# Optimization experiments

Hardware: AMD Instinct MI355X
Metric: run time of the kernel (lower is better)

Reference implementation:

```python
import jax, jax.numpy as jnp
import numpy as np

K_MSG = 1024   # message length k (rows of G)
N_CODE = 2048  # codeword length n (cols of G)
B = 32768      # number of message blocks


def setup_inputs() -> dict:
    key = jax.random.key(0)
    kb, kg = jax.random.split(key)
    b = jax.random.randint(kb, (B, K_MSG), 0, 2, dtype=jnp.int32)
    G = jax.random.randint(kg, (K_MSG, N_CODE), 0, 2, dtype=jnp.int32)
    return {"b": b, "G": G}


def reference(b, G):
    # GF(2) linear block encode: c = (b @ G) mod 2
    # b: [num_blocks, k] bits (0/1), G: [k, n] generator matrix (0/1)
    b2 = b.astype(jnp.int32)
    G2 = G.astype(jnp.int32)
    c = jnp.mod(jnp.matmul(b2, G2), 2)  # [num_blocks, n]
    return c.astype(jnp.int32)
```

## Files before the change

kernel.cpp:

```cpp
#include <hip/hip_runtime.h>
#include <stdint.h>

typedef unsigned int u32;
typedef unsigned long long u64;
typedef int v4i  __attribute__((ext_vector_type(4)));
typedef int v16i __attribute__((ext_vector_type(16)));

#define K_MSG   1024
#define N_CODE  2048
#define NB      32768

__global__ void pack_gBF(const int* __restrict__ G, u32* __restrict__ bf) {
    int idx = blockIdx.x * blockDim.x + threadIdx.x;
    const int j  = idx & (N_CODE - 1);
    const int kq = idx >> 11;
    u32 p = 0;
#pragma unroll
    for (int i = 0; i < 4; ++i) {
        int v = G[(size_t)(kq * 4 + i) * N_CODE + j];
        p |= (u32)(v & 1) << (8 * i);
    }
    const int jb = j >> 5, jr = j & 31;
    const int kb = kq >> 3, hi = (kq >> 2) & 1, b4 = kq & 3;
    bf[(size_t)(jb * 32 + kb) * 256 + hi * 128 + jr * 4 + b4] = p;
}


#define MFMA_I8(va, vb, vc) __builtin_amdgcn_mfma_i32_32x32x32_i8(va, vb, vc, 0, 0, 0)

#define MFMA_SET(sfx) do {                              \
    acc[0][0] = MFMA_I8(a0##sfx, b0##sfx, acc[0][0]);   \
    acc[0][1] = MFMA_I8(a0##sfx, b1##sfx, acc[0][1]);   \
    acc[0][2] = MFMA_I8(a0##sfx, b2##sfx, acc[0][2]);   \
    acc[0][3] = MFMA_I8(a0##sfx, b3##sfx, acc[0][3]);   \
    acc[1][0] = MFMA_I8(a1##sfx, b0##sfx, acc[1][0]);   \
    acc[1][1] = MFMA_I8(a1##sfx, b1##sfx, acc[1][1]);   \
    acc[1][2] = MFMA_I8(a1##sfx, b2##sfx, acc[1][2]);   \
    acc[1][3] = MFMA_I8(a1##sfx, b3##sfx, acc[1][3]);   \
} while (0)

#define LOAD_SET(sfx, s_) do {                                      \
    int ao_ = lr * 1024 + ((((s_) * 32) + hi * 16) ^ axor);         \
    a0##sfx = *(const v4i*)(As + ao_);                              \
    a1##sfx = *(const v4i*)(As + ao_ + 32768);                      \
    b0##sfx = *(const v4i*)(bp0 + (size_t)(s_) * 1024);             \
    b1##sfx = *(const v4i*)(bp1 + (size_t)(s_) * 1024);             \
    b2##sfx = *(const v4i*)(bp2 + (size_t)(s_) * 1024);             \
    b3##sfx = *(const v4i*)(bp3 + (size_t)(s_) * 1024);             \
} while (0)

#define EXPAND_ROW(pkp_, opp_, row_) do {                           \
    const u32 p0_ = (pkp_)[(row_) * 16 + (lane >> 3)];              \
    const u32 p1_ = (pkp_)[(row_) * 16 + 8 + (lane >> 3)];          \
    const int sb_ = (lane & 7) * 4;                                 \
    v4i v0_, v1_;                                                   \
    v0_.x = (int)((p0_ >> (sb_ + 0)) & 1u);                         \
    v0_.y = (int)((p0_ >> (sb_ + 1)) & 1u);                         \
    v0_.z = (int)((p0_ >> (sb_ + 2)) & 1u);                         \
    v0_.w = (int)((p0_ >> (sb_ + 3)) & 1u);                         \
    v1_.x = (int)((p1_ >> (sb_ + 0)) & 1u);                         \
    v1_.y = (int)((p1_ >> (sb_ + 1)) & 1u);                         \
    v1_.z = (int)((p1_ >> (sb_ + 2)) & 1u);                         \
    v1_.w = (int)((p1_ >> (sb_ + 3)) & 1u);                         \
    int* dst_ = (opp_) + (size_t)(row_) * N_CODE + lane * 4;        \
    *(v4i*)dst_         = v0_;                                      \
    *(v4i*)(dst_ + 256) = v1_;                                      \
} while (0)

__global__ __launch_bounds__(256, 2) void gemm_all(const int* __restrict__ b,
                                                   const char* __restrict__ bf,
                                                   int* __restrict__ out) {
    __shared__ __align__(16) char As[64 * 1024];
    __shared__ u32 pk[2][64 * 16];

    const int t   = threadIdx.x;
    const int bid = blockIdx.x;
    const int m0  = ((bid & 7) * 64 + (bid >> 3)) * 64;

    const int w = t >> 6, lane = t & 63, lr = lane & 31, hi = lane >> 5;
    const int axor = (lr & 7) << 4;

    {
        const int* src = b + (size_t)m0 * K_MSG;
#pragma unroll 8
        for (int i = 0; i < 64; ++i) {
            int4 v = *(const int4*)(src + (size_t)i * K_MSG + t * 4);
            u32 p = (u32)(v.x & 1) | ((u32)(v.y & 1) << 8) |
                    ((u32)(v.z & 1) << 16) | ((u32)(v.w & 1) << 24);
            *(u32*)(As + i * 1024 + ((t * 4) ^ ((i & 7) << 4))) = p;
        }
    }
    __syncthreads();

#pragma unroll 1
    for (int pass = 0; pass < 4; ++pass) {
        const int cur = pass & 1;
        const u32* pkp = pk[cur ^ 1];
        int* opp = out + (size_t)m0 * N_CODE + (pass - 1) * 512;

        const char* bp0 = bf + ((size_t)pass * 16 + w * 4) * 32768 + lane * 16;
        const char* bp1 = bp0 + 32768;
        const char* bp2 = bp0 + 65536;
        const char* bp3 = bp0 + 98304;

        v16i acc[2][4] = {};
        v4i a0A, a1A, b0A, b1A, b2A, b3A;
        v4i a0B, a1B, b0B, b1B, b2B, b3B;
        v4i a0C, a1C, b0C, b1C, b2C, b3C;
        v4i a0D, a1D, b0D, b1D, b2D, b3D;

        LOAD_SET(A, 0);
        LOAD_SET(B, 1);
#pragma unroll 1
        for (int s = 0; s < 32; s += 4) {
            LOAD_SET(C, s + 2);
            LOAD_SET(D, s + 3);
            MFMA_SET(A);
            MFMA_SET(B);
            if (s + 4 < 32) {
                LOAD_SET(A, s + 4);
                LOAD_SET(B, s + 5);
            }
            MFMA_SET(C);
            MFMA_SET(D);
            if (pass > 0) {
                const int row0 = w * 16 + (s >> 1);
                EXPAND_ROW(pkp, opp, row0);
                EXPAND_ROW(pkp, opp, row0 + 1);
            }
        }

        u32* pkc = pk[cur];
#pragma unroll
        for (int mi = 0; mi < 2; ++mi) {
#pragma unroll
            for (int ni = 0; ni < 4; ++ni) {
                const int cbL = w * 4 + ni;
#pragma unroll
                for (int r = 0; r < 16; ++r) {
                    u64 m = __ballot((acc[mi][ni][r] & 1) != 0);
                    if ((lane & 31) == r) {
                        const int row = mi * 32 + (r & 3) + 8 * (r >> 2) + 4 * hi;
                        pkc[row * 16 + cbL] = (u32)(m >> (hi * 32));
                    }
                }
            }
        }
        __syncthreads();
    }

    {
        const u32* pkp = pk[1];
        int* opp = out + (size_t)m0 * N_CODE + 3 * 512;
#pragma unroll 4
        for (int rr = 0; rr < 16; ++rr) {
            const int row = w * 16 + rr;
            EXPAND_ROW(pkp, opp, row);
        }
    }
}

__global__ void encode_naive(const int* __restrict__ b, const int* __restrict__ G,
                             int* __restrict__ out) {
    size_t idx = (size_t)blockIdx.x * blockDim.x + threadIdx.x;
    size_t total = (size_t)NB * N_CODE;
    if (idx >= total) return;
    int i = (int)(idx / N_CODE);
    int j = (int)(idx % N_CODE);
    int acc = 0;
    for (int k = 0; k < K_MSG; ++k)
        acc ^= b[(size_t)i * K_MSG + k] & G[(size_t)k * N_CODE + j];
    out[idx] = acc & 1;
}

extern "C" void kernel_launch(void* const* d_in, const int* in_sizes, int n_in,
                              void* d_out, int out_size, void* d_ws, size_t ws_size,
                              hipStream_t stream) {
    const int* b = (const int*)d_in[0];
    const int* G = (const int*)d_in[1];
    int* out = (int*)d_out;

    const size_t bf_bytes = (size_t)N_CODE * K_MSG;

    if (ws_size < bf_bytes) {
        size_t total = (size_t)NB * N_CODE;
        encode_naive<<<(unsigned)((total + 255) / 256), 256, 0, stream>>>(b, G, out);
        return;
    }

    char* bf = (char*)d_ws;

    pack_gBF<<<2048, 256, 0, stream>>>(G, (u32*)bf);
    gemm_all<<<NB / 64, 256, 0, stream>>>(b, bf, out);
}
```

Measured before the change: 134.6 us.

## Split N work across eight waves per block with smaller per-wave tiles

Doubles the block to 512 threads so each wave computes a 64x64 output slice instead of 64x128, halving accumulator and operand registers per wave. The main loop shrinks from quad-buffered to double-buffered loads, and the A staging and bit-expansion output work are redistributed across the eight waves. The aim is more resident waves to hide memory and MFMA latency. The cost is less A-fragment reuse per wave, hence more LDS reads per MFMA, and shallower software pipelining.

```diff
diff --git a/kernel.cpp b/kernel.cpp
--- a/kernel.cpp
+++ b/kernel.cpp
@@ -28,25 +28,19 @@
 
 #define MFMA_I8(va, vb, vc) __builtin_amdgcn_mfma_i32_32x32x32_i8(va, vb, vc, 0, 0, 0)
 
-#define MFMA_SET(sfx) do {                              \
+#define MFMAS(sfx) do {                                 \
     acc[0][0] = MFMA_I8(a0##sfx, b0##sfx, acc[0][0]);   \
     acc[0][1] = MFMA_I8(a0##sfx, b1##sfx, acc[0][1]);   \
-    acc[0][2] = MFMA_I8(a0##sfx, b2##sfx, acc[0][2]);   \
-    acc[0][3] = MFMA_I8(a0##sfx, b3##sfx, acc[0][3]);   \
     acc[1][0] = MFMA_I8(a1##sfx, b0##sfx, acc[1][0]);   \
     acc[1][1] = MFMA_I8(a1##sfx, b1##sfx, acc[1][1]);   \
-    acc[1][2] = MFMA_I8(a1##sfx, b2##sfx, acc[1][2]);   \
-    acc[1][3] = MFMA_I8(a1##sfx, b3##sfx, acc[1][3]);   \
 } while (0)
 
-#define LOAD_SET(sfx, s_) do {                                      \
+#define LOADS(sfx, s_) do {                                         \
     int ao_ = lr * 1024 + ((((s_) * 32) + hi * 16) ^ axor);         \
     a0##sfx = *(const v4i*)(As + ao_);                              \
     a1##sfx = *(const v4i*)(As + ao_ + 32768);                      \
     b0##sfx = *(const v4i*)(bp0 + (size_t)(s_) * 1024);             \
     b1##sfx = *(const v4i*)(bp1 + (size_t)(s_) * 1024);             \
-    b2##sfx = *(const v4i*)(bp2 + (size_t)(s_) * 1024);             \
-    b3##sfx = *(const v4i*)(bp3 + (size_t)(s_) * 1024);             \
 } while (0)
 
 #define EXPAND_ROW(pkp_, opp_, row_) do {                           \
@@ -67,7 +61,7 @@
     *(v4i*)(dst_ + 256) = v1_;                                      \
 } while (0)
 
-__global__ __launch_bounds__(256, 2) void gemm_all(const int* __restrict__ b,
+__global__ __launch_bounds__(512, 4) void gemm_all(const int* __restrict__ b,
                                                    const char* __restrict__ bf,
                                                    int* __restrict__ out) {
     __shared__ __align__(16) char As[64 * 1024];
@@ -83,11 +77,13 @@
     {
         const int* src = b + (size_t)m0 * K_MSG;
 #pragma unroll 8
-        for (int i = 0; i < 64; ++i) {
-            int4 v = *(const int4*)(src + (size_t)i * K_MSG + t * 4);
+        for (int i2 = 0; i2 < 32; ++i2) {
+            const int i  = i2 * 2 + (t >> 8);
+            const int c4 = (t & 255) * 4;
+            int4 v = *(const int4*)(src + (size_t)i * K_MSG + c4);
             u32 p = (u32)(v.x & 1) | ((u32)(v.y & 1) << 8) |
                     ((u32)(v.z & 1) << 16) | ((u32)(v.w & 1) << 24);
-            *(u32*)(As + i * 1024 + ((t * 4) ^ ((i & 7) << 4))) = p;
+            *(u32*)(As + i * 1024 + (c4 ^ ((i & 7) << 4))) = p;
         }
     }
     __syncthreads();
@@ -98,35 +94,22 @@
         const u32* pkp = pk[cur ^ 1];
         int* opp = out + (size_t)m0 * N_CODE + (pass - 1) * 512;
 
-        const char* bp0 = bf + ((size_t)pass * 16 + w * 4) * 32768 + lane * 16;
+        const char* bp0 = bf + ((size_t)pass * 16 + w * 2) * 32768 + lane * 16;
         const char* bp1 = bp0 + 32768;
-        const char* bp2 = bp0 + 65536;
-        const char* bp3 = bp0 + 98304;
 
-        v16i acc[2][4] = {};
-        v4i a0A, a1A, b0A, b1A, b2A, b3A;
-        v4i a0B, a1B, b0B, b1B, b2B, b3B;
-        v4i a0C, a1C, b0C, b1C, b2C, b3C;
-        v4i a0D, a1D, b0D, b1D, b2D, b3D;
+        v16i acc[2][2] = {};
+        v4i a0A, a1A, b0A, b1A;
+        v4i a0B, a1B, b0B, b1B;
 
-        LOAD_SET(A, 0);
-        LOAD_SET(B, 1);
+        LOADS(A, 0);
 #pragma unroll 1
-        for (int s = 0; s < 32; s += 4) {
-            LOAD_SET(C, s + 2);
-            LOAD_SET(D, s + 3);
-            MFMA_SET(A);
-            MFMA_SET(B);
-            if (s + 4 < 32) {
-                LOAD_SET(A, s + 4);
-                LOAD_SET(B, s + 5);
-            }
-            MFMA_SET(C);
-            MFMA_SET(D);
-            if (pass > 0) {
-                const int row0 = w * 16 + (s >> 1);
-                EXPAND_ROW(pkp, opp, row0);
-                EXPAND_ROW(pkp, opp, row0 + 1);
+        for (int s = 0; s < 32; s += 2) {
+            LOADS(B, s + 1);
+            MFMAS(A);
+            if (s + 2 < 32) LOADS(A, s + 2);
+            MFMAS(B);
+            if (pass > 0 && (s & 3) == 0) {
+                EXPAND_ROW(pkp, opp, w * 8 + (s >> 2));
             }
         }
 
@@ -134,8 +117,8 @@
 #pragma unroll
         for (int mi = 0; mi < 2; ++mi) {
 #pragma unroll
-            for (int ni = 0; ni < 4; ++ni) {
-                const int cbL = w * 4 + ni;
+            for (int ni = 0; ni < 2; ++ni) {
+                const int cbL = w * 2 + ni;
 #pragma unroll
                 for (int r = 0; r < 16; ++r) {
                     u64 m = __ballot((acc[mi][ni][r] & 1) != 0);
@@ -152,10 +135,9 @@
     {
         const u32* pkp = pk[1];
         int* opp = out + (size_t)m0 * N_CODE + 3 * 512;
-#pragma unroll 4
-        for (int rr = 0; rr < 16; ++rr) {
-            const int row = w * 16 + rr;
-            EXPAND_ROW(pkp, opp, row);
+#pragma unroll 2
+        for (int rr = 0; rr < 8; ++rr) {
+            EXPAND_ROW(pkp, opp, w * 8 + rr);
         }
     }
 }
@@ -191,5 +173,5 @@
     char* bf = (char*)d_ws;
 
     pack_gBF<<<2048, 256, 0, stream>>>(G, (u32*)bf);
-    gemm_all<<<NB / 64, 256, 0, stream>>>(b, bf, out);
+    gemm_all<<<NB / 64, 512, 0, stream>>>(b, bf, out);
 }
```

Result: no change. 136.2 us, median of 2 (+1.2%).

## Double the M tile to 128 rows with 8 waves sharing B fragments

Applied to the files above, without the earlier changes.

Each block now covers 128 message rows with 512 threads arranged as 2x4 waves, so the packed G fragments fetched from global memory are reused across two M sub-tiles per block. The software pipeline in the k-loop is cut from four register sets to two to save VGPRs under the larger launch bound. LDS use doubles to 128KB plus the packed-bit buffers, which with launch bounds asking for 2 blocks per CU may cap occupancy. The shallower prefetch may expose more load latency.

```diff
diff --git a/kernel.cpp b/kernel.cpp
--- a/kernel.cpp
+++ b/kernel.cpp
@@ -40,7 +40,7 @@
 } while (0)
 
 #define LOAD_SET(sfx, s_) do {                                      \
-    int ao_ = lr * 1024 + ((((s_) * 32) + hi * 16) ^ axor);         \
+    int ao_ = (wm * 64 + lr) * 1024 + ((((s_) * 32) + hi * 16) ^ axor); \
     a0##sfx = *(const v4i*)(As + ao_);                              \
     a1##sfx = *(const v4i*)(As + ao_ + 32768);                      \
     b0##sfx = *(const v4i*)(bp0 + (size_t)(s_) * 1024);             \
@@ -67,27 +67,30 @@
     *(v4i*)(dst_ + 256) = v1_;                                      \
 } while (0)
 
-__global__ __launch_bounds__(256, 2) void gemm_all(const int* __restrict__ b,
+__global__ __launch_bounds__(512, 2) void gemm_all(const int* __restrict__ b,
                                                    const char* __restrict__ bf,
                                                    int* __restrict__ out) {
-    __shared__ __align__(16) char As[64 * 1024];
-    __shared__ u32 pk[2][64 * 16];
+    __shared__ __align__(16) char As[128 * 1024];
+    __shared__ u32 pk[2][128 * 16];
 
     const int t   = threadIdx.x;
     const int bid = blockIdx.x;
-    const int m0  = ((bid & 7) * 64 + (bid >> 3)) * 64;
+    const int m0  = ((bid & 7) * 32 + (bid >> 3)) * 128;
 
     const int w = t >> 6, lane = t & 63, lr = lane & 31, hi = lane >> 5;
+    const int wm = w >> 2, wn = w & 3;
     const int axor = (lr & 7) << 4;
 
     {
         const int* src = b + (size_t)m0 * K_MSG;
 #pragma unroll 8
-        for (int i = 0; i < 64; ++i) {
-            int4 v = *(const int4*)(src + (size_t)i * K_MSG + t * 4);
+        for (int i2 = 0; i2 < 64; ++i2) {
+            const int i  = i2 * 2 + (t >> 8);
+            const int c4 = (t & 255) * 4;
+            int4 v = *(const int4*)(src + (size_t)i * K_MSG + c4);
             u32 p = (u32)(v.x & 1) | ((u32)(v.y & 1) << 8) |
                     ((u32)(v.z & 1) << 16) | ((u32)(v.w & 1) << 24);
-            *(u32*)(As + i * 1024 + ((t * 4) ^ ((i & 7) << 4))) = p;
+            *(u32*)(As + i * 1024 + (c4 ^ ((i & 7) << 4))) = p;
         }
     }
     __syncthreads();
@@ -98,7 +101,7 @@
         const u32* pkp = pk[cur ^ 1];
         int* opp = out + (size_t)m0 * N_CODE + (pass - 1) * 512;
 
-        const char* bp0 = bf + ((size_t)pass * 16 + w * 4) * 32768 + lane * 16;
+        const char* bp0 = bf + ((size_t)pass * 16 + wn * 4) * 32768 + lane * 16;
         const char* bp1 = bp0 + 32768;
         const char* bp2 = bp0 + 65536;
         const char* bp3 = bp0 + 98304;
@@ -106,27 +109,16 @@
         v16i acc[2][4] = {};
         v4i a0A, a1A, b0A, b1A, b2A, b3A;
         v4i a0B, a1B, b0B, b1B, b2B, b3B;
-        v4i a0C, a1C, b0C, b1C, b2C, b3C;
-        v4i a0D, a1D, b0D, b1D, b2D, b3D;
 
         LOAD_SET(A, 0);
-        LOAD_SET(B, 1);
 #pragma unroll 1
-        for (int s = 0; s < 32; s += 4) {
-            LOAD_SET(C, s + 2);
-            LOAD_SET(D, s + 3);
+        for (int s = 0; s < 32; s += 2) {
+            LOAD_SET(B, s + 1);
             MFMA_SET(A);
+            if (s + 2 < 32) LOAD_SET(A, s + 2);
             MFMA_SET(B);
-            if (s + 4 < 32) {
-                LOAD_SET(A, s + 4);
-                LOAD_SET(B, s + 5);
-            }
-            MFMA_SET(C);
-            MFMA_SET(D);
             if (pass > 0) {
-                const int row0 = w * 16 + (s >> 1);
-                EXPAND_ROW(pkp, opp, row0);
-                EXPAND_ROW(pkp, opp, row0 + 1);
+                EXPAND_ROW(pkp, opp, w * 16 + (s >> 1));
             }
         }
 
@@ -135,12 +127,12 @@
         for (int mi = 0; mi < 2; ++mi) {
 #pragma unroll
             for (int ni = 0; ni < 4; ++ni) {
-                const int cbL = w * 4 + ni;
+                const int cbL = wn * 4 + ni;
 #pragma unroll
                 for (int r = 0; r < 16; ++r) {
                     u64 m = __ballot((acc[mi][ni][r] & 1) != 0);
                     if ((lane & 31) == r) {
-                        const int row = mi * 32 + (r & 3) + 8 * (r >> 2) + 4 * hi;
+                        const int row = wm * 64 + mi * 32 + (r & 3) + 8 * (r >> 2) + 4 * hi;
                         pkc[row * 16 + cbL] = (u32)(m >> (hi * 32));
                     }
                 }
@@ -154,8 +146,7 @@
         int* opp = out + (size_t)m0 * N_CODE + 3 * 512;
 #pragma unroll 4
         for (int rr = 0; rr < 16; ++rr) {
-            const int row = w * 16 + rr;
-            EXPAND_ROW(pkp, opp, row);
+            EXPAND_ROW(pkp, opp, w * 16 + rr);
         }
     }
 }
@@ -191,5 +182,5 @@
     char* bf = (char*)d_ws;
 
     pack_gBF<<<2048, 256, 0, stream>>>(G, (u32*)bf);
-    gemm_all<<<NB / 64, 256, 0, stream>>>(b, bf, out);
+    gemm_all<<<NB / 128, 512, 0, stream>>>(b, bf, out);
 }
```

Result: slower. 146.6 us (+8.9%).
